# Kernel tuning notes

Hardware: AMD Instinct MI355X
Metric: run time of the kernel (lower is better)

## Reference

```python
import jax, jax.numpy as jnp
import numpy as np

B, S, D_IN, D_QK, D_V = 4, 4096, 1024, 64, 64

def setup_inputs() -> dict:
    key = jax.random.key(0)
    ks = jax.random.split(key, 8)
    sd = 1.0 / np.sqrt(D_IN)
    return {
        "X": jax.random.normal(ks[0], (B, S, D_IN), dtype=jnp.float32),
        "mask": jnp.ones((B, S, 1), dtype=jnp.float32),
        "Wq": jax.random.uniform(ks[1], (D_IN, D_QK), jnp.float32, -sd, sd),
        "bq": jax.random.uniform(ks[2], (D_QK,), jnp.float32, -sd, sd),
        "Wk": jax.random.uniform(ks[3], (D_IN, D_QK), jnp.float32, -sd, sd),
        "bk": jax.random.uniform(ks[4], (D_QK,), jnp.float32, -sd, sd),
        "Wv": jax.random.uniform(ks[5], (D_IN, D_V), jnp.float32, -sd, sd),
        "bv": jax.random.uniform(ks[6], (D_V,), jnp.float32, -sd, sd),
    }

def reference(X, mask, Wq, bq, Wk, bk, Wv, bv):
    # ReLU-activated projections (no head split, no 1/sqrt(d) scaling)
    q = jax.nn.relu(jnp.einsum('bsd,df->bsf', X, Wq) + bq)   # [B,S,D_QK]
    k = jax.nn.relu(jnp.einsum('bsd,df->bsf', X, Wk) + bk)   # [B,S,D_QK]
    v = jax.nn.relu(jnp.einsum('bsd,df->bsf', X, Wv) + bv)   # [B,S,D_V]
    scores = jax.nn.softmax(jnp.einsum('bqf,bkf->bqk', q, k), axis=-1)  # [B,S,S]
    return jnp.einsum('bqk,bkf->bqf', scores, v) * mask       # mask applied AFTER AV
```

## Files before the change

### kernel.cpp

```cpp
#include <hip/hip_runtime.h>


typedef short s16x8 __attribute__((ext_vector_type(8)));
typedef _Float16 f16x8 __attribute__((ext_vector_type(8)));
typedef float fx4   __attribute__((ext_vector_type(4)));
typedef unsigned short u16x4 __attribute__((ext_vector_type(4)));

#define LOG2E 1.4426950408889634f

__device__ __forceinline__ unsigned short f2bf(float x) {
    unsigned int u = __float_as_uint(x);
    u += 0x7FFFu + ((u >> 16) & 1u);
    return (unsigned short)(u >> 16);
}
__device__ __forceinline__ float bf2f(unsigned short b) {
    return __uint_as_float(((unsigned int)b) << 16);
}

__global__ __launch_bounds__(256) void prep_w_kernel(
    const float* __restrict__ Wq, const float* __restrict__ Wk, const float* __restrict__ Wv,
    _Float16* __restrict__ wt_h)
{
    __shared__ __align__(16) _Float16 sh[64][72];

    const int y  = blockIdx.x;
    const int kt = blockIdx.y;
    const float* W = (y == 0) ? Wq : (y == 1) ? Wk : Wv;
    const int t  = threadIdx.x;

    const int kl = t >> 2;
    const int c0 = (t & 3) * 16;
    const float* src = W + (size_t)(kt * 64 + kl) * 64 + c0;
    #pragma unroll
    for (int j = 0; j < 4; j++) {
        fx4 v = *(const fx4*)(src + j * 4);
        #pragma unroll
        for (int i = 0; i < 4; i++)
            sh[c0 + j * 4 + i][kl] = (_Float16)v[i];
    }
    __syncthreads();

    const int c  = t >> 2;
    const int k0 = (t & 3) * 16;
    size_t o = (size_t)(y * 64 + c) * 1024 + kt * 64 + k0;
    *(f16x8*)(wt_h + o)     = *(const f16x8*)&sh[c][k0];
    *(f16x8*)(wt_h + o + 8) = *(const f16x8*)&sh[c][k0 + 8];
}

__global__ __launch_bounds__(256, 4) void proj_kernel(
    const float* __restrict__ X,
    const _Float16* __restrict__ wt_h,
    const float* __restrict__ bq, const float* __restrict__ bk, const float* __restrict__ bv,
    unsigned short* __restrict__ q_hi, unsigned short* __restrict__ q_lo,
    unsigned short* __restrict__ k_bf, unsigned short* __restrict__ vt_g)
{
    __shared__ __align__(16) _Float16 wls[64][264];

    const int tid  = threadIdx.x;
    const int lane = tid & 63;
    const int w    = tid >> 6;
    const int quad = lane >> 4;
    const int l15  = lane & 15;

    const int f   = blockIdx.x;
    const int xcd = f & 7;
    const int jj  = f >> 3;
    const int y   = jj % 3;
    const int m0  = ((jj / 3) * 8 + xcd) * 64;

    const int row = m0 + w * 16 + l15;
    const float* xbase = X + (size_t)row * 1024;

    const int wcol = tid >> 2;
    const int wk0  = (tid & 3) * 64;
    const size_t wgb = (size_t)(y * 64 + wcol) * 1024 + wk0;

    f16x8 wr[8];
    #pragma unroll
    for (int i = 0; i < 8; i++)
        wr[i] = *(const f16x8*)(wt_h + wgb + i * 8);

    fx4 xc[2][2];
    #pragma unroll
    for (int ks = 0; ks < 2; ks++) {
        xc[ks][0] = *(const fx4*)(xbase + ks * 32 + quad * 8);
        xc[ks][1] = *(const fx4*)(xbase + ks * 32 + quad * 8 + 4);
    }

    fx4 acc[4];
    #pragma unroll
    for (int nt = 0; nt < 4; nt++) acc[nt] = (fx4){0.f, 0.f, 0.f, 0.f};

    for (int ch = 0; ch < 4; ch++) {
        if (ch) __syncthreads();
        #pragma unroll
        for (int i = 0; i < 8; i++)
            *(f16x8*)&wls[wcol][wk0 + i * 8] = wr[i];
        __syncthreads();
        if (ch < 3) {
            #pragma unroll
            for (int i = 0; i < 8; i++)
                wr[i] = *(const f16x8*)(wt_h + wgb + (ch + 1) * 256 + i * 8);
        }

        #pragma unroll
        for (int kk = 0; kk < 4; kk++) {
            const int kc = ch * 4 + kk;
            fx4 xn[2][2];
            if (kc < 15) {
                #pragma unroll
                for (int ks = 0; ks < 2; ks++) {
                    xn[ks][0] = *(const fx4*)(xbase + (kc + 1) * 64 + ks * 32 + quad * 8);
                    xn[ks][1] = *(const fx4*)(xbase + (kc + 1) * 64 + ks * 32 + quad * 8 + 4);
                }
            }
            f16x8 ah[2];
            #pragma unroll
            for (int ks = 0; ks < 2; ks++)
                #pragma unroll
                for (int j = 0; j < 2; j++) {
                    fx4 v = xc[ks][j];
                    #pragma unroll
                    for (int i = 0; i < 4; i++)
                        ah[ks][j * 4 + i] = (_Float16)v[i];
                }
            #pragma unroll
            for (int nt = 0; nt < 4; nt++) {
                #pragma unroll
                for (int ks = 0; ks < 2; ks++) {
                    const int ko = kk * 64 + ks * 32 + quad * 8;
                    f16x8 bh = *(const f16x8*)&wls[nt * 16 + l15][ko];
                    acc[nt] = __builtin_amdgcn_mfma_f32_16x16x32_f16(ah[ks], bh, acc[nt], 0, 0, 0);
                }
            }
            #pragma unroll
            for (int ks = 0; ks < 2; ks++) {
                xc[ks][0] = xn[ks][0];
                xc[ks][1] = xn[ks][1];
            }
        }
    }
    __syncthreads();

    const float* bias = (y == 0) ? bq : (y == 1) ? bk : bv;
    const int b   = m0 >> 12;
    const int s0b = m0 & 4095;
    unsigned short* vtr = (unsigned short*)&wls[0][0];

    #pragma unroll
    for (int nt = 0; nt < 4; nt++) {
        int col = nt * 16 + l15;
        float bb = bias[col];
        int rloc = w * 16 + quad * 4;
        #pragma unroll
        for (int r = 0; r < 4; r++) {
            float v = acc[nt][r] + bb;
            v = fmaxf(v, 0.f);
            size_t grow = (size_t)(m0 + rloc + r);
            if (y == 0) {
                unsigned short h = f2bf(v);
                unsigned short l = f2bf(v - bf2f(h));
                q_hi[grow * 64 + col] = h;
                q_lo[grow * 64 + col] = l;
            } else if (y == 1) {
                k_bf[grow * 64 + col] = f2bf(v);
            } else {
                vtr[col * 72 + rloc + r] = f2bf(v);
            }
        }
    }
    if (y == 2) {
        __syncthreads();
        int rowd = tid >> 2;
        int off  = (tid & 3) * 16;
        s16x8 v0 = *(const s16x8*)&vtr[rowd * 72 + off];
        s16x8 v1 = *(const s16x8*)&vtr[rowd * 72 + off + 8];
        *(s16x8*)(vt_g + (size_t)(b * 64 + rowd) * 4096 + s0b + off)     = v0;
        *(s16x8*)(vt_g + (size_t)(b * 64 + rowd) * 4096 + s0b + off + 8) = v1;
    }
}

__global__ __launch_bounds__(256, 6) void attn_kernel(
    const unsigned short* __restrict__ q_hi, const unsigned short* __restrict__ q_lo,
    const unsigned short* __restrict__ k_bf, const unsigned short* __restrict__ vt_g,
    unsigned short* __restrict__ pOb, float* __restrict__ pL)
{
    __shared__ __align__(16) unsigned short kt[64][72];
    __shared__ __align__(16) unsigned short vt[64][72];
    __shared__ __align__(16) unsigned short pt[4][16][40];

    const int tid  = threadIdx.x;
    const int lane = tid & 63;
    const int w    = tid >> 6;
    const int quad = lane >> 4;
    const int l15  = lane & 15;
    const int ck   = blockIdx.y;
    const int b    = blockIdx.z;
    const int q0   = blockIdx.x * 64;

    const size_t qoff = ((size_t)b * 4096 + q0 + w * 16 + l15) * 64 + quad * 8;
    s16x8 qh0 = *(const s16x8*)(q_hi + qoff);
    s16x8 qh1 = *(const s16x8*)(q_hi + qoff + 32);
    s16x8 ql0 = *(const s16x8*)(q_lo + qoff);
    s16x8 ql1 = *(const s16x8*)(q_lo + qoff + 32);

    fx4 accO[4];
    #pragma unroll
    for (int nt = 0; nt < 4; nt++) accO[nt] = (fx4){0.f, 0.f, 0.f, 0.f};
    float lsum[4] = {0.f, 0.f, 0.f, 0.f};

    const unsigned short* kgb = k_bf + (size_t)b * 4096 * 64;
    const unsigned short* vgb = vt_g + (size_t)b * 64 * 4096;

    const int srow = tid >> 3;
    const int soff = (tid & 7) * 8;

    s16x8 kr[2], vr[2];
    {
        const unsigned short* kg = kgb + (size_t)(ck * 8) * 4096;
        #pragma unroll
        for (int i = 0; i < 2; i++) {
            int row = srow + i * 32;
            kr[i] = *(const s16x8*)(kg + (size_t)row * 64 + soff);
            vr[i] = *(const s16x8*)(vgb + (size_t)row * 4096 + (ck * 8) * 64 + soff);
        }
    }

    for (int i2 = 0; i2 < 8; i2++) {
        const int it = ck * 8 + i2;
        if (i2) __syncthreads();
        #pragma unroll
        for (int i = 0; i < 2; i++) {
            int row = srow + i * 32;
            *(s16x8*)&kt[row][soff] = kr[i];
            *(s16x8*)&vt[row][soff] = vr[i];
        }
        __syncthreads();
        if (i2 < 7) {
            const unsigned short* kg = kgb + (size_t)(it + 1) * 4096;
            #pragma unroll
            for (int i = 0; i < 2; i++) {
                int row = srow + i * 32;
                kr[i] = *(const s16x8*)(kg + (size_t)row * 64 + soff);
                vr[i] = *(const s16x8*)(vgb + (size_t)row * 4096 + (it + 1) * 64 + soff);
            }
        }

        #pragma unroll
        for (int kh = 0; kh < 2; kh++) {
            #pragma unroll
            for (int nt2 = 0; nt2 < 2; nt2++) {
                int key = kh * 32 + nt2 * 16 + l15;
                s16x8 k0 = *(const s16x8*)&kt[key][quad * 8];
                s16x8 k1 = *(const s16x8*)&kt[key][32 + quad * 8];
                fx4 sc = (fx4){0.f, 0.f, 0.f, 0.f};
                sc = __builtin_amdgcn_mfma_f32_16x16x32_bf16(qh0, k0, sc, 0, 0, 0);
                sc = __builtin_amdgcn_mfma_f32_16x16x32_bf16(ql0, k0, sc, 0, 0, 0);
                sc = __builtin_amdgcn_mfma_f32_16x16x32_bf16(qh1, k1, sc, 0, 0, 0);
                sc = __builtin_amdgcn_mfma_f32_16x16x32_bf16(ql1, k1, sc, 0, 0, 0);
                #pragma unroll
                for (int r = 0; r < 4; r++) {
                    float p = __builtin_amdgcn_exp2f(sc[r] * LOG2E);
                    unsigned short pb = f2bf(p);
                    lsum[r] += bf2f(pb);
                    pt[w][quad * 4 + r][nt2 * 16 + l15] = pb;
                }
            }
            s16x8 pa = *(const s16x8*)&pt[w][l15][quad * 8];
            #pragma unroll
            for (int nt = 0; nt < 4; nt++) {
                s16x8 vf = *(const s16x8*)&vt[nt * 16 + l15][kh * 32 + quad * 8];
                accO[nt] = __builtin_amdgcn_mfma_f32_16x16x32_bf16(pa, vf, accO[nt], 0, 0, 0);
            }
        }
    }

    #pragma unroll
    for (int r = 0; r < 4; r++) {
        float v = lsum[r];
        #pragma unroll
        for (int o = 1; o < 16; o <<= 1) v += __shfl_xor(v, o);
        lsum[r] = v;
    }
    #pragma unroll
    for (int r = 0; r < 4; r++) {
        int qrow = q0 + w * 16 + quad * 4 + r;
        size_t grow = (size_t)b * 4096 + qrow;
        #pragma unroll
        for (int nt = 0; nt < 4; nt++)
            pOb[((size_t)ck * 16384 + grow) * 64 + nt * 16 + l15] = f2bf(accO[nt][r]);
        if (l15 == 0)
            pL[(size_t)ck * 16384 + grow] = lsum[r];
    }
}

__global__ __launch_bounds__(256) void combine_kernel(
    const unsigned short* __restrict__ pOb, const float* __restrict__ pL,
    const float* __restrict__ mask, float* __restrict__ out)
{
    int idx = blockIdx.x * 256 + threadIdx.x;
    int q  = idx >> 4;
    int dg = idx & 15;
    fx4 s = (fx4){0.f, 0.f, 0.f, 0.f};
    float l = 0.f;
    #pragma unroll
    for (int c = 0; c < 8; c++) {
        u16x4 h = *(const u16x4*)(pOb + ((size_t)c * 16384 + q) * 64 + dg * 4);
        s.x += bf2f(h.x);
        s.y += bf2f(h.y);
        s.z += bf2f(h.z);
        s.w += bf2f(h.w);
        l += pL[(size_t)c * 16384 + q];
    }
    float scale = mask[q] / l;
    *(fx4*)(out + (size_t)q * 64 + dg * 4) = s * scale;
}

extern "C" void kernel_launch(void* const* d_in, const int* in_sizes, int n_in,
                              void* d_out, int out_size, void* d_ws, size_t ws_size,
                              hipStream_t stream)
{
    const float* X    = (const float*)d_in[0];
    const float* mask = (const float*)d_in[1];
    const float* Wq   = (const float*)d_in[2];
    const float* bq   = (const float*)d_in[3];
    const float* Wk   = (const float*)d_in[4];
    const float* bk   = (const float*)d_in[5];
    const float* Wv   = (const float*)d_in[6];
    const float* bv   = (const float*)d_in[7];
    float* out = (float*)d_out;

    char* ws = (char*)d_ws;
    unsigned short* q_hi  = (unsigned short*)(ws);
    unsigned short* q_lo  = (unsigned short*)(ws + (size_t)(2u << 20));
    unsigned short* k_bf  = (unsigned short*)(ws + (size_t)(4u << 20));
    unsigned short* vt_g  = (unsigned short*)(ws + (size_t)(6u << 20));
    _Float16*       wt_h  = (_Float16*)(ws + (size_t)(8u << 20));
    unsigned short* pOb   = (unsigned short*)(ws + (size_t)(9u << 20));
    float*          pL    = (float*)(ws + (size_t)(25u << 20));

    hipLaunchKernelGGL(prep_w_kernel, dim3(3, 16), dim3(256), 0, stream,
                       Wq, Wk, Wv, wt_h);
    hipLaunchKernelGGL(proj_kernel, dim3(768), dim3(256), 0, stream,
                       X, wt_h, bq, bk, bv, q_hi, q_lo, k_bf, vt_g);
    hipLaunchKernelGGL(attn_kernel, dim3(64, 8, 4), dim3(256), 0, stream,
                       q_hi, q_lo, k_bf, vt_g, pOb, pL);
    hipLaunchKernelGGL(combine_kernel, dim3(1024), dim3(256), 0, stream,
                       pOb, pL, mask, out);
}
```

Measured before the change: 177.7 us.

## Pre-convert X to tiled fp16 in prep kernel and tile V layout

The weight-prep kernel now also converts X from fp32 into fp16, stored in a tiled layout of 64-row by 64-column blocks. The projection kernel then loads ready-made fp16 MFMA operands instead of reading fp32 rows and converting them in registers, which halves the bytes each of its three passes over X reads. V is also written in 64x64 tiles, so the attention kernel's V loads become contiguous per key block. The cost is an extra full pass over X plus a 32 MB fp16 intermediate, which overlaps the workspace region later reused for partial outputs.

```diff
diff --git a/kernel.cpp b/kernel.cpp
--- a/kernel.cpp
+++ b/kernel.cpp
@@ -17,39 +17,67 @@
     return __uint_as_float(((unsigned int)b) << 16);
 }
 
-__global__ __launch_bounds__(256) void prep_w_kernel(
+__global__ __launch_bounds__(256) void prep_kernel(
+    const float* __restrict__ X,
     const float* __restrict__ Wq, const float* __restrict__ Wk, const float* __restrict__ Wv,
-    _Float16* __restrict__ wt_h)
+    _Float16* __restrict__ wt_h, _Float16* __restrict__ xt)
 {
     __shared__ __align__(16) _Float16 sh[64][72];
-
-    const int y  = blockIdx.x;
-    const int kt = blockIdx.y;
-    const float* W = (y == 0) ? Wq : (y == 1) ? Wk : Wv;
-    const int t  = threadIdx.x;
-
-    const int kl = t >> 2;
-    const int c0 = (t & 3) * 16;
-    const float* src = W + (size_t)(kt * 64 + kl) * 64 + c0;
-    #pragma unroll
-    for (int j = 0; j < 4; j++) {
-        fx4 v = *(const fx4*)(src + j * 4);
-        #pragma unroll
-        for (int i = 0; i < 4; i++)
-            sh[c0 + j * 4 + i][kl] = (_Float16)v[i];
-    }
-    __syncthreads();
-
-    const int c  = t >> 2;
-    const int k0 = (t & 3) * 16;
-    size_t o = (size_t)(y * 64 + c) * 1024 + kt * 64 + k0;
-    *(f16x8*)(wt_h + o)     = *(const f16x8*)&sh[c][k0];
-    *(f16x8*)(wt_h + o + 8) = *(const f16x8*)&sh[c][k0 + 8];
+    const int bid = blockIdx.x;
+    const int t   = threadIdx.x;
+
+    if (bid < 48) {
+        const int y  = bid >> 4;
+        const int kt = bid & 15;
+        const float* W = (y == 0) ? Wq : (y == 1) ? Wk : Wv;
+
+        const int kl = t >> 2;
+        const int c0 = (t & 3) * 16;
+        const float* src = W + (size_t)(kt * 64 + kl) * 64 + c0;
+        #pragma unroll
+        for (int j = 0; j < 4; j++) {
+            fx4 v = *(const fx4*)(src + j * 4);
+            #pragma unroll
+            for (int i = 0; i < 4; i++)
+                sh[c0 + j * 4 + i][kl] = (_Float16)v[i];
+        }
+        __syncthreads();
+
+        const int c  = t >> 2;
+        const int k0 = (t & 3) * 16;
+        size_t o = (size_t)(y * 64 + c) * 1024 + kt * 64 + k0;
+        *(f16x8*)(wt_h + o)     = *(const f16x8*)&sh[c][k0];
+        *(f16x8*)(wt_h + o + 8) = *(const f16x8*)&sh[c][k0 + 8];
+    } else {
+        const int xb   = bid - 48;
+        const int tile = xb >> 2;
+        const int qrt  = xb & 3;
+        const int rl   = t >> 6;
+        const int c    = (t & 63) * 16;
+        const int kc   = c >> 6;
+        const int kk   = c & 63;
+
+        #pragma unroll
+        for (int it = 0; it < 4; it++) {
+            int row = qrt * 16 + it * 4 + rl;
+            const float* src = X + (((size_t)(tile * 64 + row)) << 10) + c;
+            _Float16 h[16];
+            #pragma unroll
+            for (int j = 0; j < 4; j++) {
+                fx4 v = *(const fx4*)(src + j * 4);
+                #pragma unroll
+                for (int i = 0; i < 4; i++)
+                    h[j * 4 + i] = (_Float16)v[i];
+            }
+            _Float16* dst = xt + ((((size_t)tile * 16 + kc) * 64 + row) << 6) + kk;
+            *(f16x8*)dst       = *(const f16x8*)&h[0];
+            *(f16x8*)(dst + 8) = *(const f16x8*)&h[8];
+        }
+    }
 }
 
 __global__ __launch_bounds__(256, 4) void proj_kernel(
-    const float* __restrict__ X,
-    const _Float16* __restrict__ wt_h,
+    const _Float16* __restrict__ xt, const _Float16* __restrict__ wt_h,
     const float* __restrict__ bq, const float* __restrict__ bk, const float* __restrict__ bv,
     unsigned short* __restrict__ q_hi, unsigned short* __restrict__ q_lo,
     unsigned short* __restrict__ k_bf, unsigned short* __restrict__ vt_g)
@@ -66,10 +94,10 @@
     const int xcd = f & 7;
     const int jj  = f >> 3;
     const int y   = jj % 3;
-    const int m0  = ((jj / 3) * 8 + xcd) * 64;
-
-    const int row = m0 + w * 16 + l15;
-    const float* xbase = X + (size_t)row * 1024;
+    const int mt  = (jj / 3) * 8 + xcd;
+    const int m0  = mt * 64;
+
+    const _Float16* xtb = xt + (((size_t)mt * 16) * 64 + (w * 16 + l15)) * 64 + quad * 8;
 
     const int wcol = tid >> 2;
     const int wk0  = (tid & 3) * 64;
@@ -80,12 +108,8 @@
     for (int i = 0; i < 8; i++)
         wr[i] = *(const f16x8*)(wt_h + wgb + i * 8);
 
-    fx4 xc[2][2];
-    #pragma unroll
-    for (int ks = 0; ks < 2; ks++) {
-        xc[ks][0] = *(const fx4*)(xbase + ks * 32 + quad * 8);
-        xc[ks][1] = *(const fx4*)(xbase + ks * 32 + quad * 8 + 4);
-    }
+    f16x8 xc0 = *(const f16x8*)(xtb);
+    f16x8 xc1 = *(const f16x8*)(xtb + 32);
 
     fx4 acc[4];
     #pragma unroll
@@ -106,45 +130,26 @@
         #pragma unroll
         for (int kk = 0; kk < 4; kk++) {
             const int kc = ch * 4 + kk;
-            fx4 xn[2][2];
+            f16x8 xn0, xn1;
             if (kc < 15) {
-                #pragma unroll
-                for (int ks = 0; ks < 2; ks++) {
-                    xn[ks][0] = *(const fx4*)(xbase + (kc + 1) * 64 + ks * 32 + quad * 8);
-                    xn[ks][1] = *(const fx4*)(xbase + (kc + 1) * 64 + ks * 32 + quad * 8 + 4);
-                }
-            }
-            f16x8 ah[2];
-            #pragma unroll
-            for (int ks = 0; ks < 2; ks++)
-                #pragma unroll
-                for (int j = 0; j < 2; j++) {
-                    fx4 v = xc[ks][j];
-                    #pragma unroll
-                    for (int i = 0; i < 4; i++)
-                        ah[ks][j * 4 + i] = (_Float16)v[i];
-                }
+                xn0 = *(const f16x8*)(xtb + (kc + 1) * 4096);
+                xn1 = *(const f16x8*)(xtb + (kc + 1) * 4096 + 32);
+            }
             #pragma unroll
             for (int nt = 0; nt < 4; nt++) {
-                #pragma unroll
-                for (int ks = 0; ks < 2; ks++) {
-                    const int ko = kk * 64 + ks * 32 + quad * 8;
-                    f16x8 bh = *(const f16x8*)&wls[nt * 16 + l15][ko];
-                    acc[nt] = __builtin_amdgcn_mfma_f32_16x16x32_f16(ah[ks], bh, acc[nt], 0, 0, 0);
-                }
-            }
-            #pragma unroll
-            for (int ks = 0; ks < 2; ks++) {
-                xc[ks][0] = xn[ks][0];
-                xc[ks][1] = xn[ks][1];
-            }
+                const int ko = kk * 64 + quad * 8;
+                f16x8 b0 = *(const f16x8*)&wls[nt * 16 + l15][ko];
+                f16x8 b1 = *(const f16x8*)&wls[nt * 16 + l15][ko + 32];
+                acc[nt] = __builtin_amdgcn_mfma_f32_16x16x32_f16(xc0, b0, acc[nt], 0, 0, 0);
+                acc[nt] = __builtin_amdgcn_mfma_f32_16x16x32_f16(xc1, b1, acc[nt], 0, 0, 0);
+            }
+            xc0 = xn0; xc1 = xn1;
         }
     }
     __syncthreads();
 
     const float* bias = (y == 0) ? bq : (y == 1) ? bk : bv;
-    const int b   = m0 >> 12;
-    const int s0b = m0 & 4095;
+
     unsigned short* vtr = (unsigned short*)&wls[0][0];
 
     #pragma unroll
@@ -175,8 +180,9 @@
         int off  = (tid & 3) * 16;
         s16x8 v0 = *(const s16x8*)&vtr[rowd * 72 + off];
         s16x8 v1 = *(const s16x8*)&vtr[rowd * 72 + off + 8];
-        *(s16x8*)(vt_g + (size_t)(b * 64 + rowd) * 4096 + s0b + off)     = v0;
-        *(s16x8*)(vt_g + (size_t)(b * 64 + rowd) * 4096 + s0b + off + 8) = v1;
+        unsigned short* dst = vt_g + ((size_t)mt * 64 + rowd) * 64 + off;
+        *(s16x8*)(dst)     = v0;
+        *(s16x8*)(dst + 8) = v1;
     }
 }
 
@@ -217,12 +223,14 @@
 
     s16x8 kr[2], vr[2];
     {
-        const unsigned short* kg = kgb + (size_t)(ck * 8) * 4096;
+        const int it0 = ck * 8;
+        const unsigned short* kg = kgb + (size_t)it0 * 4096;
+        const unsigned short* vg = vgb + (size_t)it0 * 4096;
         #pragma unroll
         for (int i = 0; i < 2; i++) {
             int row = srow + i * 32;
             kr[i] = *(const s16x8*)(kg + (size_t)row * 64 + soff);
-            vr[i] = *(const s16x8*)(vgb + (size_t)row * 4096 + (ck * 8) * 64 + soff);
+            vr[i] = *(const s16x8*)(vg + (size_t)row * 64 + soff);
         }
     }
 
@@ -238,11 +246,12 @@
         __syncthreads();
         if (i2 < 7) {
             const unsigned short* kg = kgb + (size_t)(it + 1) * 4096;
+            const unsigned short* vg = vgb + (size_t)(it + 1) * 4096;
             #pragma unroll
             for (int i = 0; i < 2; i++) {
                 int row = srow + i * 32;
                 kr[i] = *(const s16x8*)(kg + (size_t)row * 64 + soff);
-                vr[i] = *(const s16x8*)(vgb + (size_t)row * 4096 + (it + 1) * 64 + soff);
+                vr[i] = *(const s16x8*)(vg + (size_t)row * 64 + soff);
             }
         }
 
@@ -336,13 +345,14 @@
     unsigned short* k_bf  = (unsigned short*)(ws + (size_t)(4u << 20));
     unsigned short* vt_g  = (unsigned short*)(ws + (size_t)(6u << 20));
     _Float16*       wt_h  = (_Float16*)(ws + (size_t)(8u << 20));
+    _Float16*       xt    = (_Float16*)(ws + (size_t)(9u << 20));
     unsigned short* pOb   = (unsigned short*)(ws + (size_t)(9u << 20));
-    float*          pL    = (float*)(ws + (size_t)(25u << 20));
-
-    hipLaunchKernelGGL(prep_w_kernel, dim3(3, 16), dim3(256), 0, stream,
-                       Wq, Wk, Wv, wt_h);
+    float*          pL    = (float*)(ws + (size_t)(41u << 20));
+
+    hipLaunchKernelGGL(prep_kernel, dim3(1072), dim3(256), 0, stream,
+                       X, Wq, Wk, Wv, wt_h, xt);
     hipLaunchKernelGGL(proj_kernel, dim3(768), dim3(256), 0, stream,
-                       X, wt_h, bq, bk, bv, q_hi, q_lo, k_bf, vt_g);
+                       xt, wt_h, bq, bk, bv, q_hi, q_lo, k_bf, vt_g);
     hipLaunchKernelGGL(attn_kernel, dim3(64, 8, 4), dim3(256), 0, stream,
                        q_hi, q_lo, k_bf, vt_g, pOb, pL);
     hipLaunchKernelGGL(combine_kernel, dim3(1024), dim3(256), 0, stream,
```

Measured after the change: 179.4 us. About the same (+1.0%).
